# Kernel tuning notes

Hardware: AMD Instinct MI355X
Metric: run time of the kernel (lower is better)

## Reference

```python
import jax, jax.numpy as jnp
import numpy as np

LR = 0.1  # inner-loop learning rate from `param - 0.1 * grad`

D = 4096          # memory width d; key/val are (1, d) per docstring
CTX = 512         # loss_context_size: number of keys per update step


def setup_inputs() -> dict:
    key = jax.random.key(0)
    k1, k2, k3 = jax.random.split(key, 3)
    W = jax.random.normal(k1, (D, D), dtype=jnp.float32) / np.sqrt(D)
    keys = jax.random.normal(k2, (CTX, D), dtype=jnp.float32)
    vals = jax.random.normal(k3, (CTX, D), dtype=jnp.float32)
    return {"W": W, "keys": keys, "vals": vals}


def reference(W, keys, vals):
    # OneStep.forward: preds_i = functional_forward(key_i, (W,)) = key_i @ W,
    # loss = MSE(preds, vals); new_W = W - 0.1 * dloss/dW.
    # The per-key loop is batched into a single (CTX, D) x (D, D) matmul.
    def loss_fn(Wp):
        preds = keys @ Wp  # (CTX, D)
        return jnp.mean((preds - vals) ** 2)

    g = jax.grad(loss_fn)(W)
    return W - LR * g
```

## Files before the change

kernel.cpp:

```cpp
#include <hip/hip_runtime.h>
#include <hip/hip_bf16.h>


typedef __bf16 bf16_t;
typedef __bf16 bf16x8 __attribute__((ext_vector_type(8)));
typedef float f32x4 __attribute__((ext_vector_type(4)));

#define D_DIM 4096
#define CTX_N 512
#define UPD_SCALE 9.5367431640625e-8f

__device__ __forceinline__ void gld16(const bf16_t* g, bf16_t* l) {
    __builtin_amdgcn_global_load_lds(
        (const __attribute__((address_space(1))) void*)g,
        (__attribute__((address_space(3))) void*)l, 16, 0, 0);
}

__device__ __forceinline__ void t_body2(
    float* tile, const float* __restrict__ src, bf16_t* __restrict__ dstT,
    bf16_t* __restrict__ dstN, int M, int N, int bx, int by)
{
    const int tid = threadIdx.x;
    const int C0 = bx * 64, R0 = by * 64;
    const int r  = tid >> 2, cs = (tid & 3) * 16;

    const float* s = src + (size_t)(R0 + r) * N + C0 + cs;
    float f[16];
#pragma unroll
    for (int u = 0; u < 4; ++u) {
        const float4 v = ((const float4*)s)[u];
        f[4 * u + 0] = v.x; f[4 * u + 1] = v.y; f[4 * u + 2] = v.z; f[4 * u + 3] = v.w;
    }
#pragma unroll
    for (int u = 0; u < 16; ++u) tile[r * 65 + cs + u] = f[u];

    if (dstN) {
        bf16x8 v0, v1;
#pragma unroll
        for (int u = 0; u < 8; ++u) { v0[u] = (bf16_t)f[u]; v1[u] = (bf16_t)f[8 + u]; }
        bf16_t* d = dstN + (size_t)(R0 + r) * N + C0 + cs;
        *(bf16x8*)d = v0; *(bf16x8*)(d + 8) = v1;
    }
    __syncthreads();

    bf16x8 o0, o1;
#pragma unroll
    for (int u = 0; u < 8; ++u) {
        o0[u] = (bf16_t)tile[(cs + u) * 65 + r];
        o1[u] = (bf16_t)tile[(cs + 8 + u) * 65 + r];
    }
    bf16_t* d = dstT + (size_t)(C0 + r) * M + R0 + cs;
    *(bf16x8*)d = o0; *(bf16x8*)(d + 8) = o1;
}

__global__ __launch_bounds__(256) void t_all(
    const float* __restrict__ W, const float* __restrict__ K,
    const float* __restrict__ V, bf16_t* __restrict__ Wt,
    bf16_t* __restrict__ Kt, bf16_t* __restrict__ Kb, bf16_t* __restrict__ Vt)
{
    __shared__ float tile[64 * 65];
    const int y = blockIdx.y;
    if (y < 64)      t_body2(tile, W, Wt, nullptr, D_DIM, D_DIM, blockIdx.x, y);
    else if (y < 72) t_body2(tile, K, Kt, Kb,      CTX_N, D_DIM, blockIdx.x, y - 64);
    else             t_body2(tile, V, Vt, nullptr, CTX_N, D_DIM, blockIdx.x, y - 72);
}



#define K1_COMPUTE(BSEL, WA, WB)                                             \
    {                                                                        \
        const bf16_t* As = (const bf16_t*)(reg + (BSEL) * 8192);             \
        const bf16_t* Bs = (const bf16_t*)(reg + 4096 + (BSEL) * 8192);      \
        __builtin_amdgcn_s_waitcnt(WA);                                      \
        bf16x8 af[4];                                                        \
        _Pragma("unroll")                                                    \
        for (int mi = 0; mi < 4; ++mi)                                       \
            af[mi] = *(const bf16x8*)(As + (mi * 16 + l15) * 32 + quad * 8); \
        __builtin_amdgcn_s_waitcnt(WB);                                      \
        bf16x8 bq[4];                                                        \
        _Pragma("unroll")                                                    \
        for (int ni = 0; ni < 4; ++ni)                                       \
            bq[ni] = *(const bf16x8*)(Bs + (ni * 16 + l15) * 32 + quad * 8); \
        _Pragma("unroll")                                                    \
        for (int mi = 0; mi < 4; ++mi)                                       \
            _Pragma("unroll")                                                \
            for (int ni = 0; ni < 4; ++ni)                                   \
                acc[mi][ni] = __builtin_amdgcn_mfma_f32_16x16x32_bf16(       \
                    af[mi], bq[ni], acc[mi][ni], 0, 0, 0);                   \
    }

__global__ __launch_bounds__(256) void k1_residual(
    const bf16_t* __restrict__ Wt, const bf16_t* __restrict__ Kb,
    const bf16_t* __restrict__ Vt, bf16_t* __restrict__ Rt)
{
    __shared__ __align__(16) char smem[65536];

    const int tid = threadIdx.x, wave = tid >> 6, lane = tid & 63;
    const int j0 = blockIdx.x * 64, c0 = blockIdx.y * 64;
    const int l15 = lane & 15, quad = lane >> 4;
    const int kw = wave * 1024;

    char* reg = smem + wave * 16384;

    f32x4 acc[4][4] = {};

    const int srow = lane >> 2, sseg = (lane & 3) * 8;
    const bf16_t* ga = Wt + (size_t)(j0 + srow) * D_DIM + kw + sseg;
    const bf16_t* gb = Kb + (size_t)(c0 + srow) * D_DIM + kw + sseg;

    auto stageA = [&](int bsel, int ko) {
        bf16_t* la = (bf16_t*)(reg + bsel * 8192) + lane * 8;
#pragma unroll
        for (int c = 0; c < 4; ++c)
            gld16(ga + ko + (size_t)(c * 16) * D_DIM, la + c * 512);
    };
    auto stageB = [&](int bsel, int ko) {
        bf16_t* lb = (bf16_t*)(reg + 4096 + bsel * 8192) + lane * 8;
#pragma unroll
        for (int c = 0; c < 4; ++c)
            gld16(gb + ko + (size_t)(c * 16) * D_DIM, lb + c * 512);
    };

    stageA(0, 0); stageB(0, 0);
#pragma unroll 1
    for (int t = 1; t <= 29; t += 2) {
        stageA(1, t * 32); stageB(1, t * 32);
        __builtin_amdgcn_sched_barrier(0);
        K1_COMPUTE(0, 0x0f7c, 0x0f78);
        stageA(0, (t + 1) * 32); stageB(0, (t + 1) * 32);
        __builtin_amdgcn_sched_barrier(0);
        K1_COMPUTE(1, 0x0f7c, 0x0f78);
    }
    stageA(1, 31 * 32); stageB(1, 31 * 32);
    __builtin_amdgcn_sched_barrier(0);
    K1_COMPUTE(0, 0x0f7c, 0x0f78);
    K1_COMPUTE(1, 0x0f74, 0x0f70);

    float* ep = (float*)smem;
    __syncthreads();
#pragma unroll
    for (int w = 0; w < 4; ++w) {
        if (wave == w) {
#pragma unroll
            for (int mi = 0; mi < 4; ++mi)
#pragma unroll
                for (int ni = 0; ni < 4; ++ni)
#pragma unroll
                    for (int r = 0; r < 4; ++r) {
                        const int row = mi * 16 + quad * 4 + r;
                        const int col = ni * 16 + l15;
                        if (w == 0) ep[row * 68 + col]  = acc[mi][ni][r];
                        else        ep[row * 68 + col] += acc[mi][ni][r];
                    }
        }
        __syncthreads();
    }

    {
        const int row = tid >> 2, cs = (tid & 3) * 16;
        const size_t rbase = (size_t)(j0 + row) * CTX_N + c0 + cs;
        float e[16];
#pragma unroll
        for (int u = 0; u < 4; ++u) {
            const float4 v = ((const float4*)(ep + row * 68 + cs))[u];
            e[4 * u + 0] = v.x; e[4 * u + 1] = v.y;
            e[4 * u + 2] = v.z; e[4 * u + 3] = v.w;
        }
        const bf16x8 v0 = *(const bf16x8*)(Vt + rbase);
        const bf16x8 v1 = *(const bf16x8*)(Vt + rbase + 8);
        bf16x8 o0, o1;
#pragma unroll
        for (int u = 0; u < 8; ++u) {
            o0[u] = (bf16_t)(e[u]     - (float)v0[u]);
            o1[u] = (bf16_t)(e[8 + u] - (float)v1[u]);
        }
        *(bf16x8*)(Rt + rbase)     = o0;
        *(bf16x8*)(Rt + rbase + 8) = o1;
    }
}


#define K2_COMPUTE(BSEL)                                                     \
    {                                                                        \
        const bf16_t* As = (const bf16_t*)(smem + (BSEL) * 16384);           \
        const bf16_t* Bs = (const bf16_t*)(smem + (BSEL) * 16384 + 8192);    \
        bf16x8 af[4], bq[4];                                                 \
        _Pragma("unroll")                                                    \
        for (int mi = 0; mi < 4; ++mi)                                       \
            af[mi] = *(const bf16x8*)(As + (wi + mi * 16 + l15) * 32 + quad * 8); \
        _Pragma("unroll")                                                    \
        for (int ni = 0; ni < 4; ++ni)                                       \
            bq[ni] = *(const bf16x8*)(Bs + (wj + ni * 16 + l15) * 32 + quad * 8); \
        _Pragma("unroll")                                                    \
        for (int mi = 0; mi < 4; ++mi)                                       \
            _Pragma("unroll")                                                \
            for (int ni = 0; ni < 4; ++ni)                                   \
                acc[mi][ni] = __builtin_amdgcn_mfma_f32_16x16x32_bf16(       \
                    af[mi], bq[ni], acc[mi][ni], 0, 0, 0);                   \
    }

__global__ __launch_bounds__(256) void k2_update(
    const bf16_t* __restrict__ Kt, const bf16_t* __restrict__ Rt,
    const float* __restrict__ W, float* __restrict__ out)
{
    __shared__ __align__(16) char smem[32768];

    const int tid = threadIdx.x;
    const int j0 = blockIdx.x * 128, i0 = blockIdx.y * 128;
    const int lane = tid & 63, wave = tid >> 6;
    const int wi = (wave >> 1) * 64, wj = (wave & 1) * 64;
    const int l15 = lane & 15, quad = lane >> 4;

    f32x4 acc[4][4] = {};

    const bf16_t* ga = Kt + (size_t)(i0 + (tid >> 2)) * CTX_N + (tid & 3) * 8;
    const bf16_t* gb = Rt + (size_t)(j0 + (tid >> 2)) * CTX_N + (tid & 3) * 8;

    auto stage = [&](int bsel, int cc) {
        bf16_t* la = (bf16_t*)(smem + bsel * 16384) + tid * 8;
        bf16_t* lb = (bf16_t*)(smem + bsel * 16384 + 8192) + tid * 8;
        gld16(ga + cc, la);
        gld16(ga + cc + (size_t)64 * CTX_N, la + 64 * 32);
        gld16(gb + cc, lb);
        gld16(gb + cc + (size_t)64 * CTX_N, lb + 64 * 32);
    };

    stage(0, 0);
    __syncthreads();
#pragma unroll 1
    for (int t = 1; t <= 13; t += 2) {
        stage(1, t * 32);
        __builtin_amdgcn_sched_barrier(0);
        K2_COMPUTE(0);
        __syncthreads();
        stage(0, (t + 1) * 32);
        __builtin_amdgcn_sched_barrier(0);
        K2_COMPUTE(1);
        __syncthreads();
    }
    stage(1, 15 * 32);
    __builtin_amdgcn_sched_barrier(0);
    K2_COMPUTE(0);
    __syncthreads();
    K2_COMPUTE(1);
    __syncthreads();

    float* ep = (float*)smem;
    const int row = tid >> 3;
    const int cb  = (tid & 7) * 16;
#pragma unroll
    for (int p = 0; p < 4; ++p) {
        const float* wrow = W + (size_t)(i0 + p * 32 + row) * D_DIM + j0 + cb;
        float4 wv[4];
#pragma unroll
        for (int u = 0; u < 4; ++u) wv[u] = ((const float4*)wrow)[u];

        if ((wave >> 1) == (p >> 1)) {
#pragma unroll
            for (int mh = 0; mh < 2; ++mh) {
                const int mi = (p & 1) * 2 + mh;
#pragma unroll
                for (int ni = 0; ni < 4; ++ni)
#pragma unroll
                    for (int r = 0; r < 4; ++r)
                        ep[(mh * 16 + quad * 4 + r) * 132 + wj + ni * 16 + l15] =
                            acc[mi][ni][r];
            }
        }
        __syncthreads();
        {
            float* orow = out + (size_t)(i0 + p * 32 + row) * D_DIM + j0 + cb;
            const float* erow = ep + row * 132 + cb;
#pragma unroll
            for (int u = 0; u < 4; ++u) {
                const float4 ev = ((const float4*)erow)[u];
                float4 ov;
                ov.x = wv[u].x - UPD_SCALE * ev.x;
                ov.y = wv[u].y - UPD_SCALE * ev.y;
                ov.z = wv[u].z - UPD_SCALE * ev.z;
                ov.w = wv[u].w - UPD_SCALE * ev.w;
                ((float4*)orow)[u] = ov;
            }
        }
        __syncthreads();
    }
}

extern "C" void kernel_launch(void* const* d_in, const int* in_sizes, int n_in,
                              void* d_out, int out_size, void* d_ws, size_t ws_size,
                              hipStream_t stream) {
    const float* W = (const float*)d_in[0];
    const float* K = (const float*)d_in[1];
    const float* V = (const float*)d_in[2];
    float* out = (float*)d_out;

    char* ws = (char*)d_ws;
    bf16_t* Wt = (bf16_t*)(ws);
    bf16_t* Kt = (bf16_t*)(ws + (size_t)32 * 1024 * 1024);
    bf16_t* Kb = (bf16_t*)(ws + (size_t)36 * 1024 * 1024);
    bf16_t* Vt = (bf16_t*)(ws + (size_t)40 * 1024 * 1024);
    bf16_t* Rt = (bf16_t*)(ws + (size_t)44 * 1024 * 1024);

    t_all      <<<dim3(64, 80), 256, 0, stream>>>(W, K, V, Wt, Kt, Kb, Vt);
    k1_residual<<<dim3(64, 8),  256, 0, stream>>>(Wt, Kb, Vt, Rt);
    k2_update  <<<dim3(32, 32), 256, 0, stream>>>(Kt, Rt, W, out);
}
```

Baseline: 206.5 us.

## Write update epilogue directly from MFMA registers and swizzle block order

The epilogue no longer stages accumulators through shared memory with barriers. Each lane now reads W and writes out directly at its MFMA fragment positions, double-buffering the W loads one fragment row ahead. Block IDs are also remapped into groups of eight rows so that neighbouring blocks share operand tiles in cache. In exchange, the global accesses become scalar 4-byte loads and stores spread over 16-lane segments per row instead of float4 rows, which may reduce coalescing efficiency.

```diff
diff --git a/kernel.cpp b/kernel.cpp
--- a/kernel.cpp
+++ b/kernel.cpp
@@ -206,7 +206,12 @@
     __shared__ __align__(16) char smem[32768];
 
     const int tid = threadIdx.x;
-    const int j0 = blockIdx.x * 128, i0 = blockIdx.y * 128;
+
+    const int id = blockIdx.x + 32 * blockIdx.y;
+    const int xp = (id >> 3) & 31;
+    const int yp = (id & 7) + 8 * (id >> 8);
+    const int j0 = xp * 128, i0 = yp * 128;
+
     const int lane = tid & 63, wave = tid >> 6;
     const int wi = (wave >> 1) * 64, wj = (wave & 1) * 64;
     const int l15 = lane & 15, quad = lane >> 4;
@@ -243,46 +248,36 @@
     K2_COMPUTE(0);
     __syncthreads();
     K2_COMPUTE(1);
-    __syncthreads();
-
-    float* ep = (float*)smem;
-    const int row = tid >> 3;
-    const int cb  = (tid & 7) * 16;
-#pragma unroll
-    for (int p = 0; p < 4; ++p) {
-        const float* wrow = W + (size_t)(i0 + p * 32 + row) * D_DIM + j0 + cb;
-        float4 wv[4];
-#pragma unroll
-        for (int u = 0; u < 4; ++u) wv[u] = ((const float4*)wrow)[u];
-
-        if ((wave >> 1) == (p >> 1)) {
-#pragma unroll
-            for (int mh = 0; mh < 2; ++mh) {
-                const int mi = (p & 1) * 2 + mh;
+
+    const size_t base = (size_t)(i0 + wi + quad * 4) * D_DIM + j0 + wj + l15;
+    const float* wp = W + base;
+    float*       op = out + base;
+
+    float w0[16], w1[16];
+#pragma unroll
+    for (int r = 0; r < 4; ++r)
+#pragma unroll
+        for (int ni = 0; ni < 4; ++ni)
+            w0[r * 4 + ni] = wp[(size_t)r * D_DIM + ni * 16];
+
+#pragma unroll
+    for (int mi = 0; mi < 4; ++mi) {
+        float* wcur = (mi & 1) ? w1 : w0;
+        float* wnxt = (mi & 1) ? w0 : w1;
+        if (mi < 3) {
+#pragma unroll
+            for (int r = 0; r < 4; ++r)
 #pragma unroll
                 for (int ni = 0; ni < 4; ++ni)
-#pragma unroll
-                    for (int r = 0; r < 4; ++r)
-                        ep[(mh * 16 + quad * 4 + r) * 132 + wj + ni * 16 + l15] =
-                            acc[mi][ni][r];
-            }
+                    wnxt[r * 4 + ni] =
+                        wp[(size_t)((mi + 1) * 16 + r) * D_DIM + ni * 16];
         }
-        __syncthreads();
-        {
-            float* orow = out + (size_t)(i0 + p * 32 + row) * D_DIM + j0 + cb;
-            const float* erow = ep + row * 132 + cb;
-#pragma unroll
-            for (int u = 0; u < 4; ++u) {
-                const float4 ev = ((const float4*)erow)[u];
-                float4 ov;
-                ov.x = wv[u].x - UPD_SCALE * ev.x;
-                ov.y = wv[u].y - UPD_SCALE * ev.y;
-                ov.z = wv[u].z - UPD_SCALE * ev.z;
-                ov.w = wv[u].w - UPD_SCALE * ev.w;
-                ((float4*)orow)[u] = ov;
-            }
-        }
-        __syncthreads();
+#pragma unroll
+        for (int r = 0; r < 4; ++r)
+#pragma unroll
+            for (int ni = 0; ni < 4; ++ni)
+                op[(size_t)(mi * 16 + r) * D_DIM + ni * 16] =
+                    wcur[r * 4 + ni] - UPD_SCALE * acc[mi][ni][r];
     }
 }
 
```

Result: faster. 199.7 us (-3.3%).
